# Optimization experiments

Measured on AMD Instinct MI355X. Metric: run time of the kernel, lower is better.

## Reference

```python
import jax, jax.numpy as jnp
import numpy as np

B = 1024        # batch
T_HIST = 50     # history length fed to LSTM
ENC_IN = 96     # 32+32+32 (zone + person + zone embeds)
ENC_H = 128     # encoder_hidden_dim
CDE_H = 64      # cde_hidden_dim
CH = 33         # control path channels = 1 + zone_embed_dim
NZ = 10000      # num_zones
NI = 4          # spline intervals
MLP = 128       # CDEFunc hidden width
N_STEPS = 16    # fixed dopri5 steps (stand-in for adaptive dopri5)


def setup_inputs() -> dict:
    key = jax.random.key(0)
    ks = jax.random.split(key, 20)
    def w(k, shape, s=0.05):
        return jax.random.normal(k, shape, dtype=jnp.float32) * s
    return {
        "history_path": jax.random.normal(ks[0], (B, T_HIST, ENC_IN), dtype=jnp.float32),
        "cde_coeffs": jax.random.normal(ks[1], (B, NI, 4, CH), dtype=jnp.float32),
        "cde_times": jnp.arange(2, dtype=jnp.float32),
        "W_ih0": w(ks[2], (4 * ENC_H, ENC_IN)), "W_hh0": w(ks[3], (4 * ENC_H, ENC_H)),
        "b_ih0": w(ks[4], (4 * ENC_H,)), "b_hh0": w(ks[5], (4 * ENC_H,)),
        "W_ih1": w(ks[6], (4 * ENC_H, ENC_H)), "W_hh1": w(ks[7], (4 * ENC_H, ENC_H)),
        "b_ih1": w(ks[8], (4 * ENC_H,)), "b_hh1": w(ks[9], (4 * ENC_H,)),
        "W_map": w(ks[10], (CDE_H, ENC_H)), "b_map": w(ks[11], (CDE_H,)),
        "gamma": jnp.ones((CDE_H,), jnp.float32), "beta": jnp.zeros((CDE_H,), jnp.float32),
        "W1": w(ks[12], (MLP, CDE_H)), "b1": w(ks[13], (MLP,)),
        "W2": w(ks[14], (CH * CDE_H, MLP)), "b2": w(ks[15], (CH * CDE_H,)),
        "W_pred": w(ks[16], (NZ, CDE_H)), "b_pred": w(ks[17], (NZ,)),
    }


def _lstm_layer(x, Wih, Whh, bih, bhh):
    # x: (B, T, D) -> (outputs (B,T,H), final h (B,H)); torch gate order i,f,g,o
    H = Whh.shape[1]
    h0 = jnp.zeros((x.shape[0], H), x.dtype)
    c0 = jnp.zeros_like(h0)
    def step(carry, xt):
        h, c = carry
        g = xt @ Wih.T + h @ Whh.T + bih + bhh
        i, f, gg, o = jnp.split(g, 4, axis=-1)
        c = jax.nn.sigmoid(f) * c + jax.nn.sigmoid(i) * jnp.tanh(gg)
        h = jax.nn.sigmoid(o) * jnp.tanh(c)
        return (h, c), h
    (h, c), hs = jax.lax.scan(step, (h0, c0), jnp.swapaxes(x, 0, 1))
    return jnp.swapaxes(hs, 0, 1), h


def _forward(history_path, cde_coeffs, cde_times,
             W_ih0, W_hh0, b_ih0, b_hh0, W_ih1, W_hh1, b_ih1, b_hh1,
             W_map, b_map, gamma, beta, W1, b1, W2, b2, W_pred, b_pred):
    # --- LSTM encoder (2 layers, eval mode: no dropout) ---
    seq0, _ = _lstm_layer(history_path, W_ih0, W_hh0, b_ih0, b_hh0)
    _, context = _lstm_layer(seq0, W_ih1, W_hh1, b_ih1, b_hh1)
    h0 = jnp.tanh(context @ W_map.T + b_map)  # (B, CDE_H)

    t0, t1 = cde_times[0], cde_times[-1]
    n_int = cde_coeffs.shape[1]
    seg = (t1 - t0) / n_int

    def dXdt(t):
        # cubic spline derivative: X(u)=a+b*u+c*u^2+d*u^3 per interval
        idx = jnp.clip(jnp.floor((t - t0) / seg).astype(jnp.int32), 0, n_int - 1)
        u = t - (t0 + idx.astype(jnp.float32) * seg)
        cc = cde_coeffs[:, idx]  # (B, 4, CH)
        return cc[:, 1] + 2.0 * cc[:, 2] * u + 3.0 * cc[:, 3] * u * u  # (B, CH)

    def vf(t, z):
        # CDEFunc: LayerNorm -> Linear(64,128) -> ReLU -> Linear(128,2112) -> tanh
        mu = z.mean(-1, keepdims=True)
        var = ((z - mu) ** 2).mean(-1, keepdims=True)
        zn = (z - mu) / jnp.sqrt(var + 1e-5) * gamma + beta
        a = jax.nn.relu(zn @ W1.T + b1)
        f = jnp.tanh(a @ W2.T + b2).reshape(z.shape[0], CDE_H, CH)  # (B, H, CH)
        return jnp.einsum('bhi,bi->bh', f, dXdt(t))

    # --- fixed-step dopri5 (5th-order solution weights) ---
    dt = (t1 - t0) / N_STEPS
    def step(z, i):
        t = t0 + i * dt
        k1 = vf(t, z)
        k2 = vf(t + dt / 5, z + dt * (k1 / 5))
        k3 = vf(t + 3 * dt / 10, z + dt * (3 / 40 * k1 + 9 / 40 * k2))
        k4 = vf(t + 4 * dt / 5, z + dt * (44 / 45 * k1 - 56 / 15 * k2 + 32 / 9 * k3))
        k5 = vf(t + 8 * dt / 9, z + dt * (19372 / 6561 * k1 - 25360 / 2187 * k2 + 64448 / 6561 * k3 - 212 / 729 * k4))
        k6 = vf(t + dt, z + dt * (9017 / 3168 * k1 - 355 / 33 * k2 + 46732 / 5247 * k3 + 49 / 176 * k4 - 5103 / 18656 * k5))
        z = z + dt * (35 / 384 * k1 + 500 / 1113 * k3 + 125 / 192 * k4 - 2187 / 6784 * k5 + 11 / 84 * k6)
        return z, None
    z, _ = jax.lax.scan(step, h0, jnp.arange(N_STEPS, dtype=jnp.float32))

    return z @ W_pred.T + b_pred  # (B, NZ)


def reference(history_path, cde_coeffs, cde_times,
              W_ih0, W_hh0, b_ih0, b_hh0, W_ih1, W_hh1, b_ih1, b_hh1,
              W_map, b_map, gamma, beta, W1, b1, W2, b2, W_pred, b_pred):
    return _forward(history_path, cde_coeffs, cde_times,
                    W_ih0, W_hh0, b_ih0, b_hh0, W_ih1, W_hh1, b_ih1, b_hh1,
                    W_map, b_map, gamma, beta, W1, b1, W2, b2, W_pred, b_pred)
```

## Files before the change

### kernel.cpp

```cpp
#include <hip/hip_runtime.h>
#include <hip/hip_bf16.h>

typedef _Float16 f16;
typedef _Float16 f16x8 __attribute__((ext_vector_type(8)));
typedef _Float16 f16x4 __attribute__((ext_vector_type(4)));
typedef float    f32x4 __attribute__((ext_vector_type(4)));

#define MFMA(a,b,c) __builtin_amdgcn_mfma_f32_16x16x32_f16((a),(b),(c),0,0,0)

#define BATCH 1024
#define T_HIST 50
#define ENC_IN 96
#define ENC_H 128
#define G4 512
#define CDE_H 64
#define NCH 33
#define MLP_H 128
#define NZ 10000
#define NSTEP 16
#define SROWS (BATCH*T_HIST)

__device__ __forceinline__ float sigf(float x){
  return __builtin_amdgcn_rcpf(1.f + __builtin_amdgcn_exp2f(-1.44269504f*x));
}
__device__ __forceinline__ float tanhc(float x){
  return 1.f - 2.f*__builtin_amdgcn_rcpf(1.f + __builtin_amdgcn_exp2f(2.88539008f*x));
}

__global__ __launch_bounds__(256) void pack_weights(
    const float* __restrict__ wih0, const float* __restrict__ whh0,
    const float* __restrict__ wih1, const float* __restrict__ whh1,
    const float* __restrict__ w1,   const float* __restrict__ wmap,
    const float* __restrict__ w2,   const float* __restrict__ wpred,
    f16* fwih0, f16* fwhh0, f16* fwih1, f16* fwhh1,
    f16* fw1, f16* fwmap, f16* fw2, f16* fwpred)
{
  int bi = blockIdx.x;
  const float* src; f16* dst; int KK, K, n; bool perm=false;
  if      (bi < 32)  { src=wih0;  dst=fwih0;  KK=3; K=96;  n=bi; }
  else if (bi < 64)  { src=whh0;  dst=fwhh0;  KK=4; K=128; n=bi-32; }
  else if (bi < 96)  { src=wih1;  dst=fwih1;  KK=4; K=128; n=bi-64; }
  else if (bi < 128) { src=whh1;  dst=fwhh1;  KK=4; K=128; n=bi-96; }
  else if (bi < 136) { src=w1;    dst=fw1;    KK=2; K=64;  n=bi-128; }
  else if (bi < 140) { src=wmap;  dst=fwmap;  KK=4; K=128; n=bi-136; }
  else if (bi < 284) { src=w2;    dst=fw2;    KK=4; K=128; n=bi-140; perm=true; }
  else               { src=wpred; dst=fwpred; KK=2; K=64;  n=bi-284; }
  int kkI = threadIdx.x>>6, lane = threadIdx.x&63;
  if (kkI >= KK) return;
  int nout = perm ? (n + (n>>4)) : n;
  f16* o = dst + (((size_t)nout*KK + kkI)*64 + lane)*8;
  if(perm && n>=132){
    #pragma unroll
    for(int j=0;j<8;j++) o[j] = (f16)0.f;
    return;
  }
  int col = n*16 + (lane&15);
  int row = perm ? ((col&63)*NCH + (col>>6)) : col;
  int k0  = kkI*32 + (lane>>4)*8;
  const float* s = src + (size_t)row*K + k0;
  #pragma unroll
  for(int j=0;j<8;j++) o[j] = (f16)s[j];
}

__global__ __launch_bounds__(256) void gemm_g0(
    const float* __restrict__ X, const f16* __restrict__ Bf,
    const float* __restrict__ bih, const float* __restrict__ bhh,
    f16* __restrict__ G)
{
  int m = blockIdx.x;
  int w = threadIdx.x>>6, lane = threadIdx.x&63;
  int lm = lane&15, quad = lane>>4;
  int arow = m*16 + lm;
  f16x8 af[3];
  #pragma unroll
  for(int kk=0;kk<3;kk++){
    const float* p = X + (size_t)arow*ENC_IN + kk*32 + quad*8;
    f16x8 v;
    #pragma unroll
    for(int j=0;j<8;j++) v[j] = (f16)p[j];
    af[kk]=v;
  }
  const f16x8* bf8 = (const f16x8*)Bf;
  #pragma unroll
  for(int jt=0;jt<8;jt++){
    int n = w*8 + jt;
    f32x4 acc = {0.f,0.f,0.f,0.f};
    #pragma unroll
    for(int kk=0;kk<3;kk++)
      acc = MFMA(af[kk], bf8[(n*3+kk)*64 + lane], acc);
    int col = n*16 + lm;
    float bias = bih[col] + bhh[col];
    #pragma unroll
    for(int r=0;r<4;r++){
      int srow = m*16 + quad*4 + r;
      int b = srow / T_HIST, t = srow - b*T_HIST;
      G[((size_t)t*BATCH + b)*G4 + col] = (f16)(acc[r] + bias);
    }
  }
}

__global__ __launch_bounds__(256) void gemm_g1(
    const f16* __restrict__ X, const f16* __restrict__ Bf,
    const float* __restrict__ bih, const float* __restrict__ bhh,
    f16* __restrict__ G)
{
  int m = blockIdx.x;
  int w = threadIdx.x>>6, lane = threadIdx.x&63;
  int lm = lane&15, quad = lane>>4;
  int arow = m*16 + lm;
  f16x8 af[4];
  #pragma unroll
  for(int kk=0;kk<4;kk++)
    af[kk] = *(const f16x8*)(X + (size_t)arow*ENC_H + kk*32 + quad*8);
  const f16x8* bf8 = (const f16x8*)Bf;
  #pragma unroll
  for(int jt=0;jt<8;jt++){
    int n = w*8 + jt;
    f32x4 acc = {0.f,0.f,0.f,0.f};
    #pragma unroll
    for(int kk=0;kk<4;kk++)
      acc = MFMA(af[kk], bf8[(n*4+kk)*64 + lane], acc);
    int col = n*16 + lm;
    float bias = bih[col]+bhh[col];
    #pragma unroll
    for(int r=0;r<4;r++){
      int srow = m*16 + quad*4 + r;
      G[(size_t)srow*G4 + col] = (f16)(acc[r]+bias);
    }
  }
}

__global__ __launch_bounds__(512,2) void lstm_kernel(
    const f16* __restrict__ G, const f16* __restrict__ Whhf,
    f16* __restrict__ seqout,
    const f16* __restrict__ Wmapf, const float* __restrict__ bmap,
    float* __restrict__ z0, int layer)
{
  __shared__ __align__(16) f16 hbuf[16][136];
  int w = threadIdx.x>>6, lane = threadIdx.x&63;
  int lm = lane&15, quad = lane>>4;
  int row0 = blockIdx.x*16;

  const f16x8* wf8 = (const f16x8*)Whhf;
  f16x8 Bf[4][4];
  #pragma unroll
  for(int m=0;m<4;m++){
    int n = w + 8*m;
    #pragma unroll
    for(int kk=0;kk<4;kk++)
      Bf[m][kk] = wf8[(n*4+kk)*64 + lane];
  }
  for(int i=threadIdx.x;i<16*136;i+=512) ((f16*)hbuf)[i] = (f16)0.f;
  float cst[4];
  #pragma unroll
  for(int r=0;r<4;r++) cst[r]=0.f;
  __syncthreads();

  for(int t=0;t<T_HIST;t++){
    float gin[4][4];
    const f16* Gt = G + ((size_t)t*BATCH + row0)*G4;
    #pragma unroll
    for(int m=0;m<4;m++){
      int col = (w+8*m)*16 + lm;
      #pragma unroll
      for(int r=0;r<4;r++)
        gin[m][r] = (float)Gt[(quad*4+r)*G4 + col];
    }
    f16x8 af[4];
    #pragma unroll
    for(int kk=0;kk<4;kk++)
      af[kk] = *(const f16x8*)&hbuf[lm][kk*32 + quad*8];
    f32x4 acc[4];
    #pragma unroll
    for(int m=0;m<4;m++){ acc[m][0]=0.f;acc[m][1]=0.f;acc[m][2]=0.f;acc[m][3]=0.f; }
    #pragma unroll
    for(int m=0;m<4;m++){
      #pragma unroll
      for(int kk=0;kk<4;kk++)
        acc[m] = MFMA(af[kk], Bf[m][kk], acc[m]);
    }
    __syncthreads();
    int hcol = w*16 + lm;
    #pragma unroll
    for(int r=0;r<4;r++){
      float gi = acc[0][r]+gin[0][r], gf = acc[1][r]+gin[1][r];
      float gg = acc[2][r]+gin[2][r], go = acc[3][r]+gin[3][r];
      float c = sigf(gf)*cst[r] + sigf(gi)*tanhc(gg);
      float h = sigf(go)*tanhc(c);
      cst[r]=c;
      hbuf[quad*4+r][hcol] = (f16)h;
      if(layer==0)
        seqout[((size_t)t*BATCH + row0 + quad*4 + r)*ENC_H + hcol] = (f16)h;
    }
    __syncthreads();
  }
  if(layer==1 && w<4){
    f16x8 af[4];
    #pragma unroll
    for(int kk=0;kk<4;kk++)
      af[kk] = *(const f16x8*)&hbuf[lm][kk*32+quad*8];
    const f16x8* mf8 = (const f16x8*)Wmapf;
    float bm = bmap[w*16+lm];
    f32x4 acc = {bm,bm,bm,bm};
    #pragma unroll
    for(int kk=0;kk<4;kk++)
      acc = MFMA(af[kk], mf8[(w*4+kk)*64+lane], acc);
    #pragma unroll
    for(int r=0;r<4;r++)
      z0[(size_t)(row0+quad*4+r)*CDE_H + w*16+lm] = tanhc(acc[r]);
  }
}

__global__ __launch_bounds__(1024)
__attribute__((amdgpu_waves_per_eu(4,4)))
void cde_kernel(
    const float* __restrict__ z0, const float* __restrict__ coeffs,
    const float* __restrict__ times,
    const f16* __restrict__ W1f, const f16* __restrict__ W2f,
    const float* __restrict__ b1, const float* __restrict__ b2,
    const float* __restrict__ gamma_, const float* __restrict__ beta_,
    float* __restrict__ zf)
{
  __shared__ __align__(16) float kpart[4][16][68];
  __shared__ __align__(16) f16   znbuf[16][72];
  __shared__ __align__(16) f16   abuf[16][136];
  __shared__ __align__(16) float dxbuf2[36*16];
  __shared__ __align__(16) float b2lds[64*36];
  __shared__ __align__(16) float cxlds[4*528*3];
  __shared__ __align__(16) f16x8 w1lds[8*2*64];

  int tid = threadIdx.x;
  int w = tid>>6, lane = tid&63, lm = lane&15, quad = lane>>4;
  int row0 = blockIdx.x*16;
  int arow = w;

  for(int i=tid;i<8*2*64;i+=1024) w1lds[i] = ((const f16x8*)W1f)[i];
  for(int i=tid;i<64*36;i+=1024){
    int h=i/36, j=i-h*36;
    b2lds[i] = (j<NCH)? b2[h*NCH+j] : 0.f;
  }
  for(int t=tid;t<2112;t+=1024){
    int seg = t/528, rem = t-seg*528, r = rem/33, q = rem-r*33;
    const float* cc = coeffs + (((size_t)(row0+r)*4 + seg)*4)*NCH + q;
    cxlds[t*3+0] = cc[NCH];
    cxlds[t*3+1] = cc[2*NCH];
    cxlds[t*3+2] = cc[3*NCH];
  }
  if(tid<48) dxbuf2[(33+tid/16)*16 + (tid&15)] = 0.f;

  float zreg = z0[(size_t)(row0+arow)*CDE_H + lane];
  float k1=0.f,k2=0.f,k3=0.f,k4=0.f,k5=0.f;
  float gam = gamma_[lane], bet = beta_[lane];

  float t0 = times[0], t1 = times[1];
  float dt = (t1-t0)/(float)NSTEP, seg = (t1-t0)*0.25f;
  float invseg = 4.f/(t1-t0);

  int ct = tid - 512;
  int doff=0, doff2=0, ddst=0, ddst2=0;
  if(ct>=0){
    int dr = ct/NCH, dq = ct - dr*NCH;
    doff = (dr*NCH+dq)*3; ddst = dq*16+dr;
    int dq2 = 17+ct;
    doff2 = (15*NCH+dq2)*3; ddst2 = dq2*16+15;
  }
  float b1r = b1[(w&7)*16 + lm];
  int g = w>>2, ws = w&3;
  const f16x8* pw = (const f16x8*)W2f + ((size_t)(g*4+ws)*4)*64 + lane;
  int b2base = (ws*16+lm)*36 + g;
  __syncthreads();

  for(int istep=0;istep<NSTEP;istep++){
    #pragma unroll
    for(int s=0;s<6;s++){
      {
        float kprev = kpart[0][arow][lane] + kpart[1][arow][lane]
                    + kpart[2][arow][lane] + kpart[3][arow][lane];
        if(s==1) k1=kprev;
        if(s==2) k2=kprev;
        if(s==3) k3=kprev;
        if(s==4) k4=kprev;
        if(s==5) k5=kprev;
        float v = zreg;
        if(s==1) v += dt*0.2f*k1;
        if(s==2) v += dt*((float)(3.0/40.0)*k1 + (float)(9.0/40.0)*k2);
        if(s==3) v += dt*((float)(44.0/45.0)*k1 + (float)(-56.0/15.0)*k2 + (float)(32.0/9.0)*k3);
        if(s==4) v += dt*((float)(19372.0/6561.0)*k1 + (float)(-25360.0/2187.0)*k2
                        + (float)(64448.0/6561.0)*k3 + (float)(-212.0/729.0)*k4);
        if(s==5) v += dt*((float)(9017.0/3168.0)*k1 + (float)(-355.0/33.0)*k2
                        + (float)(46732.0/5247.0)*k3 + (float)(49.0/176.0)*k4
                        + (float)(-5103.0/18656.0)*k5);
        float sum = v, ssq = v*v;
        #pragma unroll
        for(int m=1;m<64;m<<=1){
          sum += __shfl_xor(sum, m);
          ssq += __shfl_xor(ssq, m);
        }
        float mu   = sum*(1.f/CDE_H);
        float var  = ssq*(1.f/CDE_H) - mu*mu;
        float rstd = rsqrtf(var + 1e-5f);
        znbuf[arow][lane] = (f16)(((v-mu)*rstd)*gam + bet);
      }
      __syncthreads();
      if(w<8){
        f16x8 af1[2];
        #pragma unroll
        for(int kk=0;kk<2;kk++)
          af1[kk] = *(const f16x8*)&znbuf[lm][kk*32+quad*8];
        f32x4 acc={0.f,0.f,0.f,0.f};
        #pragma unroll
        for(int kk=0;kk<2;kk++)
          acc = MFMA(af1[kk], w1lds[(w*2+kk)*64+lane], acc);
        int col = w*16+lm;
        #pragma unroll
        for(int r=0;r<4;r++){
          float a = acc[r]+b1r;
          abuf[quad*4+r][col] = (f16)(a>0.f? a:0.f);
        }
      } else {
        const float cC[6] = {0.f,0.2f,0.3f,0.8f,(float)(8.0/9.0),1.f};
        float ts = t0 + ((float)istep + cC[s])*dt;
        int idxt = (int)floorf((ts-t0)*invseg);
        idxt = min(3, max(0, idxt));
        float u = ts - (t0 + (float)idxt*seg);
        int base = idxt*1584;
        {
          float c1=cxlds[base+doff], c2=cxlds[base+doff+1], c3=cxlds[base+doff+2];
          dxbuf2[ddst] = c1 + u*(2.f*c2 + 3.f*c3*u);
        }
        if(ct<16){
          float c1=cxlds[base+doff2], c2=cxlds[base+doff2+1], c3=cxlds[base+doff2+2];
          dxbuf2[ddst2] = c1 + u*(2.f*c2 + 3.f*c3*u);
        }
      }
      __syncthreads();
      {
        f16x8 af2[4];
        #pragma unroll
        for(int kk=0;kk<4;kk++)
          af2[kk] = *(const f16x8*)&abuf[lm][kk*32+quad*8];
        f32x4 kacc = {0.f,0.f,0.f,0.f};
        const f16x8* p2 = pw;
        f16x8 c0 = p2[0], c1 = p2[64], c2 = p2[128], c3 = p2[192];
        #pragma unroll 1
        for(int i=0;i<8;i++){
          p2 += 4352;
          f16x8 n0 = p2[0], n1 = p2[64], n2 = p2[128], n3 = p2[192];
          float bv = b2lds[b2base + 4*i];
          f32x4 dx4 = *(const f32x4*)&dxbuf2[(g+4*i)*16 + quad*4];
          f32x4 a2 = {bv,bv,bv,bv};
          a2 = MFMA(af2[0],c0,a2);
          a2 = MFMA(af2[1],c1,a2);
          a2 = MFMA(af2[2],c2,a2);
          a2 = MFMA(af2[3],c3,a2);
          #pragma unroll
          for(int r=0;r<4;r++)
            kacc[r] += tanhc(a2[r])*dx4[r];
          c0=n0; c1=n1; c2=n2; c3=n3;
        }
        {
          float bv = b2lds[b2base + 32];
          f32x4 dx4 = *(const f32x4*)&dxbuf2[(g+32)*16 + quad*4];
          f32x4 a2 = {bv,bv,bv,bv};
          a2 = MFMA(af2[0],c0,a2);
          a2 = MFMA(af2[1],c1,a2);
          a2 = MFMA(af2[2],c2,a2);
          a2 = MFMA(af2[3],c3,a2);
          #pragma unroll
          for(int r=0;r<4;r++)
            kacc[r] += tanhc(a2[r])*dx4[r];
        }
        #pragma unroll
        for(int r=0;r<4;r++)
          kpart[g][quad*4+r][ws*16+lm] = kacc[r];
      }
      __syncthreads();
    }
    {
      float k6 = kpart[0][arow][lane] + kpart[1][arow][lane]
               + kpart[2][arow][lane] + kpart[3][arow][lane];
      zreg += dt*( (float)(35.0/384.0)*k1 + (float)(500.0/1113.0)*k3
                 + (float)(125.0/192.0)*k4 + (float)(-2187.0/6784.0)*k5
                 + (float)(11.0/84.0)*k6 );
      if(istep==NSTEP-1)
        zf[(size_t)(row0+arow)*CDE_H + lane] = zreg;
    }
  }
}

__global__ __launch_bounds__(256) void gemm_out(
    const float* __restrict__ zfin, const f16* __restrict__ Wpf,
    const float* __restrict__ bpred, float* __restrict__ out)
{
  int m = blockIdx.x, g = blockIdx.y;
  int w = threadIdx.x>>6, lane = threadIdx.x&63, lm=lane&15, quad=lane>>4;
  int arow = m*16+lm;
  f16x8 af[2];
  #pragma unroll
  for(int kk=0;kk<2;kk++){
    const float* p = zfin + (size_t)arow*CDE_H + kk*32 + quad*8;
    f16x8 v;
    #pragma unroll
    for(int j=0;j<8;j++) v[j]=(f16)p[j];
    af[kk]=v;
  }
  const f16x8* wp8 = (const f16x8*)Wpf;
  #pragma unroll
  for(int jt=0;jt<4;jt++){
    int n = g*16 + w*4 + jt;
    if(n >= NZ/16) break;
    f32x4 acc={0.f,0.f,0.f,0.f};
    #pragma unroll
    for(int kk=0;kk<2;kk++)
      acc = MFMA(af[kk], wp8[((size_t)n*2+kk)*64+lane], acc);
    int col = n*16+lm;
    float bp = bpred[col];
    #pragma unroll
    for(int r=0;r<4;r++)
      out[(size_t)(m*16+quad*4+r)*NZ + col] = acc[r]+bp;
  }
}

extern "C" void kernel_launch(void* const* d_in, const int* in_sizes, int n_in,
                              void* d_out, int out_size, void* d_ws, size_t ws_size,
                              hipStream_t stream) {
  (void)in_sizes; (void)n_in; (void)out_size; (void)ws_size;
  const float* history = (const float*)d_in[0];
  const float* coeffs  = (const float*)d_in[1];
  const float* times   = (const float*)d_in[2];
  const float* Wih0 = (const float*)d_in[3];
  const float* Whh0 = (const float*)d_in[4];
  const float* bih0 = (const float*)d_in[5];
  const float* bhh0 = (const float*)d_in[6];
  const float* Wih1 = (const float*)d_in[7];
  const float* Whh1 = (const float*)d_in[8];
  const float* bih1 = (const float*)d_in[9];
  const float* bhh1 = (const float*)d_in[10];
  const float* Wmap = (const float*)d_in[11];
  const float* bmap = (const float*)d_in[12];
  const float* gam  = (const float*)d_in[13];
  const float* bet  = (const float*)d_in[14];
  const float* W1   = (const float*)d_in[15];
  const float* b1   = (const float*)d_in[16];
  const float* W2   = (const float*)d_in[17];
  const float* b2   = (const float*)d_in[18];
  const float* Wpred= (const float*)d_in[19];
  const float* bpred= (const float*)d_in[20];
  float* out = (float*)d_out;

  char* ws = (char*)d_ws;
  size_t off=0;
  auto alloc=[&](size_t bytes)->void*{
    void* p = ws+off; off += (bytes+255)&~(size_t)255; return p;
  };
  f16* G      = (f16*)alloc((size_t)SROWS*G4*sizeof(f16));
  f16* seq0   = (f16*)alloc((size_t)SROWS*ENC_H*sizeof(f16));
  f16* fwih0  = (f16*)alloc((size_t)32*3*64*8*sizeof(f16));
  f16* fwhh0  = (f16*)alloc((size_t)32*4*64*8*sizeof(f16));
  f16* fwih1  = (f16*)alloc((size_t)32*4*64*8*sizeof(f16));
  f16* fwhh1  = (f16*)alloc((size_t)32*4*64*8*sizeof(f16));
  f16* fw1    = (f16*)alloc((size_t)8*2*64*8*sizeof(f16));
  f16* fwmap  = (f16*)alloc((size_t)4*4*64*8*sizeof(f16));
  f16* fw2    = (f16*)alloc((size_t)153*4*64*8*sizeof(f16));
  f16* fwpred = (f16*)alloc((size_t)625*2*64*8*sizeof(f16));
  float* z0   = (float*)alloc((size_t)BATCH*CDE_H*sizeof(float));
  float* zfin = (float*)alloc((size_t)BATCH*CDE_H*sizeof(float));

  pack_weights<<<909,256,0,stream>>>(Wih0,Whh0,Wih1,Whh1,W1,Wmap,W2,Wpred,
      fwih0,fwhh0,fwih1,fwhh1,fw1,fwmap,fw2,fwpred);
  gemm_g0<<<SROWS/16,256,0,stream>>>(history,fwih0,bih0,bhh0,G);
  lstm_kernel<<<64,512,0,stream>>>(G,fwhh0,seq0,fwmap,bmap,z0,0);
  gemm_g1<<<SROWS/16,256,0,stream>>>(seq0,fwih1,bih1,bhh1,G);
  lstm_kernel<<<64,512,0,stream>>>(G,fwhh1,nullptr,fwmap,bmap,z0,1);
  cde_kernel<<<64,1024,0,stream>>>(z0,coeffs,times,fw1,fw2,b1,b2,gam,bet,zfin);
  gemm_out<<<dim3(64,40),256,0,stream>>>(zfin,fwpred,bpred,out);
}
```

Measured before the change: 834.2 us.

## Interleave LSTM gate layout, double-buffer h, prefetch gates, two-chain CDE MFMA loop

The gate-projection GEMMs now write G interleaved per hidden unit (i,f,g,o contiguous), so the LSTM kernel reads one f16x4 per row instead of four scalar loads. The recurrent step gains a double-buffered h in LDS, which drops one barrier per timestep, and prefetches the next step's gates. It also splits the MFMA chains into two independent accumulators. In the CDE kernel, W2 and b2 are pre-scaled by the tanh exponent constant to save a multiply, and the inner loop runs two independent MFMA chains per iteration for more ILP. The cost is more register pressure and a small f16 rounding change from pre-scaling W2.

```diff
diff --git a/kernel.cpp b/kernel.cpp
--- a/kernel.cpp
+++ b/kernel.cpp
@@ -19,12 +19,16 @@
 #define NZ 10000
 #define NSTEP 16
 #define SROWS (BATCH*T_HIST)
+#define TSCALE 2.88539008f
 
 __device__ __forceinline__ float sigf(float x){
   return __builtin_amdgcn_rcpf(1.f + __builtin_amdgcn_exp2f(-1.44269504f*x));
 }
 __device__ __forceinline__ float tanhc(float x){
-  return 1.f - 2.f*__builtin_amdgcn_rcpf(1.f + __builtin_amdgcn_exp2f(2.88539008f*x));
+  return 1.f - 2.f*__builtin_amdgcn_rcpf(1.f + __builtin_amdgcn_exp2f(TSCALE*x));
+}
+__device__ __forceinline__ float tanhs(float y){
+  return 1.f - 2.f*__builtin_amdgcn_rcpf(1.f + __builtin_amdgcn_exp2f(y));
 }
 
 __global__ __launch_bounds__(256) void pack_weights(
@@ -58,8 +62,9 @@
   int row = perm ? ((col&63)*NCH + (col>>6)) : col;
   int k0  = kkI*32 + (lane>>4)*8;
   const float* s = src + (size_t)row*K + k0;
-  #pragma unroll
-  for(int j=0;j<8;j++) o[j] = (f16)s[j];
+  float sc = perm ? TSCALE : 1.f;
+  #pragma unroll
+  for(int j=0;j<8;j++) o[j] = (f16)(s[j]*sc);
 }
 
 __global__ __launch_bounds__(256) void gemm_g0(
@@ -67,10 +72,10 @@
     const float* __restrict__ bih, const float* __restrict__ bhh,
     f16* __restrict__ G)
 {
-  int m = blockIdx.x;
+  int mb = blockIdx.x;
   int w = threadIdx.x>>6, lane = threadIdx.x&63;
   int lm = lane&15, quad = lane>>4;
-  int arow = m*16 + lm;
+  int arow = mb*16 + lm;
   f16x8 af[3];
   #pragma unroll
   for(int kk=0;kk<3;kk++){
@@ -82,19 +87,28 @@
   }
   const f16x8* bf8 = (const f16x8*)Bf;
   #pragma unroll
-  for(int jt=0;jt<8;jt++){
-    int n = w*8 + jt;
-    f32x4 acc = {0.f,0.f,0.f,0.f};
-    #pragma unroll
-    for(int kk=0;kk<3;kk++)
-      acc = MFMA(af[kk], bf8[(n*3+kk)*64 + lane], acc);
-    int col = n*16 + lm;
-    float bias = bih[col] + bhh[col];
+  for(int ht2=0; ht2<2; ht2++){
+    int ht = 2*w + ht2;
+    f32x4 am[4]; float bs[4];
+    #pragma unroll
+    for(int mg=0; mg<4; mg++){
+      int n = 8*mg + ht;
+      f32x4 acc = {0.f,0.f,0.f,0.f};
+      #pragma unroll
+      for(int kk=0;kk<3;kk++)
+        acc = MFMA(af[kk], bf8[(n*3+kk)*64 + lane], acc);
+      am[mg] = acc;
+      bs[mg] = bih[n*16+lm] + bhh[n*16+lm];
+    }
+    int h = ht*16 + lm;
     #pragma unroll
     for(int r=0;r<4;r++){
-      int srow = m*16 + quad*4 + r;
+      int srow = mb*16 + quad*4 + r;
       int b = srow / T_HIST, t = srow - b*T_HIST;
-      G[((size_t)t*BATCH + b)*G4 + col] = (f16)(acc[r] + bias);
+      f16x4 gvv;
+      #pragma unroll
+      for(int mg=0;mg<4;mg++) gvv[mg] = (f16)(am[mg][r] + bs[mg]);
+      *(f16x4*)&G[((size_t)t*BATCH + b)*G4 + h*4] = gvv;
     }
   }
 }
@@ -104,28 +118,37 @@
     const float* __restrict__ bih, const float* __restrict__ bhh,
     f16* __restrict__ G)
 {
-  int m = blockIdx.x;
+  int mb = blockIdx.x;
   int w = threadIdx.x>>6, lane = threadIdx.x&63;
   int lm = lane&15, quad = lane>>4;
-  int arow = m*16 + lm;
+  int arow = mb*16 + lm;
   f16x8 af[4];
   #pragma unroll
   for(int kk=0;kk<4;kk++)
     af[kk] = *(const f16x8*)(X + (size_t)arow*ENC_H + kk*32 + quad*8);
   const f16x8* bf8 = (const f16x8*)Bf;
   #pragma unroll
-  for(int jt=0;jt<8;jt++){
-    int n = w*8 + jt;
-    f32x4 acc = {0.f,0.f,0.f,0.f};
-    #pragma unroll
-    for(int kk=0;kk<4;kk++)
-      acc = MFMA(af[kk], bf8[(n*4+kk)*64 + lane], acc);
-    int col = n*16 + lm;
-    float bias = bih[col]+bhh[col];
+  for(int ht2=0; ht2<2; ht2++){
+    int ht = 2*w + ht2;
+    f32x4 am[4]; float bs[4];
+    #pragma unroll
+    for(int mg=0; mg<4; mg++){
+      int n = 8*mg + ht;
+      f32x4 acc = {0.f,0.f,0.f,0.f};
+      #pragma unroll
+      for(int kk=0;kk<4;kk++)
+        acc = MFMA(af[kk], bf8[(n*4+kk)*64 + lane], acc);
+      am[mg] = acc;
+      bs[mg] = bih[n*16+lm] + bhh[n*16+lm];
+    }
+    int h = ht*16 + lm;
     #pragma unroll
     for(int r=0;r<4;r++){
-      int srow = m*16 + quad*4 + r;
-      G[(size_t)srow*G4 + col] = (f16)(acc[r]+bias);
+      int srow = mb*16 + quad*4 + r;
+      f16x4 gvv;
+      #pragma unroll
+      for(int mg=0;mg<4;mg++) gvv[mg] = (f16)(am[mg][r] + bs[mg]);
+      *(f16x4*)&G[(size_t)srow*G4 + h*4] = gvv;
     }
   }
 }
@@ -136,10 +159,11 @@
     const f16* __restrict__ Wmapf, const float* __restrict__ bmap,
     float* __restrict__ z0, int layer)
 {
-  __shared__ __align__(16) f16 hbuf[16][136];
+  __shared__ __align__(16) f16 hbuf[2][16][136];
   int w = threadIdx.x>>6, lane = threadIdx.x&63;
   int lm = lane&15, quad = lane>>4;
   int row0 = blockIdx.x*16;
+  int hcol = w*16 + lm;
 
   const f16x8* wf8 = (const f16x8*)Whhf;
   f16x8 Bf[4][4];
@@ -150,55 +174,66 @@
     for(int kk=0;kk<4;kk++)
       Bf[m][kk] = wf8[(n*4+kk)*64 + lane];
   }
-  for(int i=threadIdx.x;i<16*136;i+=512) ((f16*)hbuf)[i] = (f16)0.f;
+  for(int i=threadIdx.x;i<2*16*136;i+=512) ((f16*)hbuf)[i] = (f16)0.f;
   float cst[4];
   #pragma unroll
   for(int r=0;r<4;r++) cst[r]=0.f;
   __syncthreads();
 
+  f16x4 gv[4];
+  {
+    const f16* Gt = G + (size_t)row0*G4;
+    #pragma unroll
+    for(int r=0;r<4;r++)
+      gv[r] = *(const f16x4*)(Gt + (quad*4+r)*G4 + hcol*4);
+  }
+
   for(int t=0;t<T_HIST;t++){
-    float gin[4][4];
-    const f16* Gt = G + ((size_t)t*BATCH + row0)*G4;
+    int cur = t&1;
+    f16x8 af[4];
+    #pragma unroll
+    for(int kk=0;kk<4;kk++)
+      af[kk] = *(const f16x8*)&hbuf[cur][lm][kk*32 + quad*8];
+    f32x4 accP[4], accQ[4];
     #pragma unroll
     for(int m=0;m<4;m++){
-      int col = (w+8*m)*16 + lm;
+      f32x4 z4 = {0.f,0.f,0.f,0.f};
+      accP[m] = MFMA(af[0], Bf[m][0], z4);
+      accQ[m] = MFMA(af[2], Bf[m][2], z4);
+      accP[m] = MFMA(af[1], Bf[m][1], accP[m]);
+      accQ[m] = MFMA(af[3], Bf[m][3], accQ[m]);
+    }
+    f16x4 gn[4];
+    #pragma unroll
+    for(int r=0;r<4;r++) gn[r]=gv[r];
+    if(t+1<T_HIST){
+      const f16* Gt = G + ((size_t)(t+1)*BATCH + row0)*G4;
       #pragma unroll
       for(int r=0;r<4;r++)
-        gin[m][r] = (float)Gt[(quad*4+r)*G4 + col];
-    }
-    f16x8 af[4];
-    #pragma unroll
-    for(int kk=0;kk<4;kk++)
-      af[kk] = *(const f16x8*)&hbuf[lm][kk*32 + quad*8];
-    f32x4 acc[4];
-    #pragma unroll
-    for(int m=0;m<4;m++){ acc[m][0]=0.f;acc[m][1]=0.f;acc[m][2]=0.f;acc[m][3]=0.f; }
-    #pragma unroll
-    for(int m=0;m<4;m++){
-      #pragma unroll
-      for(int kk=0;kk<4;kk++)
-        acc[m] = MFMA(af[kk], Bf[m][kk], acc[m]);
-    }
-    __syncthreads();
-    int hcol = w*16 + lm;
+        gn[r] = *(const f16x4*)(Gt + (quad*4+r)*G4 + hcol*4);
+    }
     #pragma unroll
     for(int r=0;r<4;r++){
-      float gi = acc[0][r]+gin[0][r], gf = acc[1][r]+gin[1][r];
-      float gg = acc[2][r]+gin[2][r], go = acc[3][r]+gin[3][r];
+      float gi = accP[0][r]+accQ[0][r]+(float)gv[r][0];
+      float gf = accP[1][r]+accQ[1][r]+(float)gv[r][1];
+      float gg = accP[2][r]+accQ[2][r]+(float)gv[r][2];
+      float go = accP[3][r]+accQ[3][r]+(float)gv[r][3];
       float c = sigf(gf)*cst[r] + sigf(gi)*tanhc(gg);
       float h = sigf(go)*tanhc(c);
       cst[r]=c;
-      hbuf[quad*4+r][hcol] = (f16)h;
+      hbuf[1-cur][quad*4+r][hcol] = (f16)h;
       if(layer==0)
         seqout[((size_t)t*BATCH + row0 + quad*4 + r)*ENC_H + hcol] = (f16)h;
     }
+    #pragma unroll
+    for(int r=0;r<4;r++) gv[r]=gn[r];
     __syncthreads();
   }
   if(layer==1 && w<4){
     f16x8 af[4];
     #pragma unroll
     for(int kk=0;kk<4;kk++)
-      af[kk] = *(const f16x8*)&hbuf[lm][kk*32+quad*8];
+      af[kk] = *(const f16x8*)&hbuf[0][lm][kk*32+quad*8];
     const f16x8* mf8 = (const f16x8*)Wmapf;
     float bm = bmap[w*16+lm];
     f32x4 acc = {bm,bm,bm,bm};
@@ -237,7 +272,7 @@
   for(int i=tid;i<8*2*64;i+=1024) w1lds[i] = ((const f16x8*)W1f)[i];
   for(int i=tid;i<64*36;i+=1024){
     int h=i/36, j=i-h*36;
-    b2lds[i] = (j<NCH)? b2[h*NCH+j] : 0.f;
+    b2lds[i] = (j<NCH)? b2[h*NCH+j]*TSCALE : 0.f;
   }
   for(int t=tid;t<2112;t+=1024){
     int seg = t/528, rem = t-seg*528, r = rem/33, q = rem-r*33;
@@ -341,34 +376,41 @@
           af2[kk] = *(const f16x8*)&abuf[lm][kk*32+quad*8];
         f32x4 kacc = {0.f,0.f,0.f,0.f};
         const f16x8* p2 = pw;
-        f16x8 c0 = p2[0], c1 = p2[64], c2 = p2[128], c3 = p2[192];
+        f16x8 c00=p2[0],    c01=p2[64],      c02=p2[128],      c03=p2[192];
+        f16x8 c10=p2[4352], c11=p2[4352+64], c12=p2[4352+128], c13=p2[4352+192];
         #pragma unroll 1
-        for(int i=0;i<8;i++){
-          p2 += 4352;
-          f16x8 n0 = p2[0], n1 = p2[64], n2 = p2[128], n3 = p2[192];
-          float bv = b2lds[b2base + 4*i];
-          f32x4 dx4 = *(const f32x4*)&dxbuf2[(g+4*i)*16 + quad*4];
-          f32x4 a2 = {bv,bv,bv,bv};
-          a2 = MFMA(af2[0],c0,a2);
-          a2 = MFMA(af2[1],c1,a2);
-          a2 = MFMA(af2[2],c2,a2);
-          a2 = MFMA(af2[3],c3,a2);
+        for(int i=0;i<4;i++){
+          p2 += 8704;
+          const f16x8* q2 = (i<3) ? (p2+4352) : p2;
+          f16x8 n00=p2[0],  n01=p2[64],  n02=p2[128],  n03=p2[192];
+          f16x8 n10=q2[0],  n11=q2[64],  n12=q2[128],  n13=q2[192];
+          float bvA = b2lds[b2base + 8*i];
+          float bvB = b2lds[b2base + 8*i + 4];
+          f32x4 dxA = *(const f32x4*)&dxbuf2[(g+8*i)*16 + quad*4];
+          f32x4 dxB = *(const f32x4*)&dxbuf2[(g+8*i+4)*16 + quad*4];
+          f32x4 aA = {bvA,bvA,bvA,bvA};
+          f32x4 aB = {bvB,bvB,bvB,bvB};
+          aA = MFMA(af2[0],c00,aA); aB = MFMA(af2[0],c10,aB);
+          aA = MFMA(af2[1],c01,aA); aB = MFMA(af2[1],c11,aB);
+          aA = MFMA(af2[2],c02,aA); aB = MFMA(af2[2],c12,aB);
+          aA = MFMA(af2[3],c03,aA); aB = MFMA(af2[3],c13,aB);
           #pragma unroll
           for(int r=0;r<4;r++)
-            kacc[r] += tanhc(a2[r])*dx4[r];
-          c0=n0; c1=n1; c2=n2; c3=n3;
+            kacc[r] += tanhs(aA[r])*dxA[r] + tanhs(aB[r])*dxB[r];
+          c00=n00;c01=n01;c02=n02;c03=n03;
+          c10=n10;c11=n11;c12=n12;c13=n13;
         }
         {
           float bv = b2lds[b2base + 32];
           f32x4 dx4 = *(const f32x4*)&dxbuf2[(g+32)*16 + quad*4];
           f32x4 a2 = {bv,bv,bv,bv};
-          a2 = MFMA(af2[0],c0,a2);
-          a2 = MFMA(af2[1],c1,a2);
-          a2 = MFMA(af2[2],c2,a2);
-          a2 = MFMA(af2[3],c3,a2);
+          a2 = MFMA(af2[0],c00,a2);
+          a2 = MFMA(af2[1],c01,a2);
+          a2 = MFMA(af2[2],c02,a2);
+          a2 = MFMA(af2[3],c03,a2);
           #pragma unroll
           for(int r=0;r<4;r++)
-            kacc[r] += tanhc(a2[r])*dx4[r];
+            kacc[r] += tanhs(a2[r])*dx4[r];
         }
         #pragma unroll
         for(int r=0;r<4;r++)
```

Result: slower. 974.9 us (+16.9%).
